# Performance work log

Hardware: AMD Instinct MI355X
Metric: run time of the kernel (lower is better)

## Reference

```python
import jax, jax.numpy as jnp
import numpy as np

B, S, E, H = 2, 2048, 1024, 16
D = E // H          # head_dim = 64
HK = H // 4         # heads per kernel group = 4
MASKED_BIAS = -10000.0


def _dwconv_causal(x, w, b):
    # x: [B, h, S, D], w: [D, k], b: [D]; causal depthwise conv along S
    k = w.shape[1]
    s = x.shape[2]
    xp = jnp.pad(x, ((0, 0), (0, 0), (k - 1, 0), (0, 0)))
    out = b
    for i in range(k):
        out = out + xp[:, :, i:i + s, :] * w[:, i]
    return out


def setup_inputs() -> dict:
    key = jax.random.key(0)
    ks = jax.random.split(key, 32)
    inp = {
        'hidden_states': jax.random.normal(ks[0], (B, S, E), jnp.float32),
        'c_attn_w': jax.random.normal(ks[1], (E, 3 * E), jnp.float32) * 0.02,
        'c_attn_b': jnp.zeros((3 * E,), jnp.float32),
        'c_proj_w': jax.random.normal(ks[2], (E, E), jnp.float32) * 0.02,
        'c_proj_b': jnp.zeros((E,), jnp.float32),
    }
    i = 3
    for pre in ('q', 'k', 'v'):
        for kern in (3, 5, 7):
            inp[f'{pre}w{kern}'] = jax.random.normal(ks[i], (D, kern), jnp.float32) * (1.0 / kern)
            inp[f'{pre}b{kern}'] = jnp.zeros((D,), jnp.float32)
            i += 1
    return inp


def _forward(hidden_states, c_attn_w, c_attn_b, c_proj_w, c_proj_b,
             qw3, qb3, qw5, qb5, qw7, qb7,
             kw3, kb3, kw5, kb5, kw7, kb7,
             vw3, vb3, vw5, vb5, vw7, vb7):
    qkv = hidden_states @ c_attn_w + c_attn_b            # [B,S,3E]
    q, k, v = jnp.split(qkv, 3, axis=-1)

    def split_heads(t):
        return t.reshape(B, S, H, D).transpose(0, 2, 1, 3)  # [B,H,S,D]

    q, k, v = split_heads(q), split_heads(k), split_heads(v)

    def tranception_mix(t, ws_bs):
        parts = [t[:, :HK]]
        for g, (w, b) in enumerate(ws_bs):
            parts.append(_dwconv_causal(t[:, (g + 1) * HK:(g + 2) * HK], w, b))
        return jnp.concatenate(parts, axis=1)

    q = tranception_mix(q, [(qw3, qb3), (qw5, qb5), (qw7, qb7)])
    k = tranception_mix(k, [(kw3, kb3), (kw5, kb5), (kw7, kb7)])
    v = tranception_mix(v, [(vw3, vb3), (vw5, vb5), (vw7, vb7)])

    scores = jnp.einsum('bhqd,bhkd->bhqk', q, k) / jnp.sqrt(jnp.float32(D))
    causal = jnp.tril(jnp.ones((S, S), bool))
    scores = jnp.where(causal, scores, jnp.float32(MASKED_BIAS))
    attn = jax.nn.softmax(scores, axis=-1)
    out = jnp.einsum('bhqk,bhkd->bhqd', attn, v)
    out = out.transpose(0, 2, 1, 3).reshape(B, S, E)
    return out @ c_proj_w + c_proj_b


def reference(hidden_states, c_attn_w, c_attn_b, c_proj_w, c_proj_b,
              qw3, qb3, qw5, qb5, qw7, qb7,
              kw3, kb3, kw5, kb5, kw7, kb7,
              vw3, vb3, vw5, vb5, vw7, vb7):
    return _forward(hidden_states, c_attn_w, c_attn_b, c_proj_w, c_proj_b,
                    qw3, qb3, qw5, qb5, qw7, qb7,
                    kw3, kb3, kw5, kb5, kw7, kb7,
                    vw3, vb3, vw5, vb5, vw7, vb7)
```

## Files before the change

kernel.cpp:

```cpp
#include <hip/hip_runtime.h>
#include <stdint.h>
#include <math.h>

typedef unsigned short u16;
typedef __attribute__((ext_vector_type(8))) short short8;
typedef __attribute__((ext_vector_type(4))) float floatx4;

#define DEV static __device__ __forceinline__

struct alignas(8) us4 { u16 x, y, z, w; };
struct alignas(16) us8 { u16 v[8]; };
struct alignas(16) f4 { float x, y, z, w; };
struct alignas(8) f2 { float x, y; };
struct alignas(8) u32x2 { uint32_t x, y; };

DEV u16 f2bf(float f) {
  uint32_t u = __float_as_uint(f);
  u += 0x7fffu + ((u >> 16) & 1u);
  return (u16)(u >> 16);
}
DEV float bf2f(u16 h) { return __uint_as_float(((uint32_t)h) << 16); }

DEV uint32_t pkbf(float a, float b) {
#if __has_builtin(__builtin_amdgcn_cvt_pk_bf16_f32)
  typedef __attribute__((ext_vector_type(2))) __bf16 bf2_t;
  bf2_t v = __builtin_amdgcn_cvt_pk_bf16_f32(a, b);
  uint32_t r; __builtin_memcpy(&r, &v, 4); return r;
#else
  return (uint32_t)f2bf(a) | ((uint32_t)f2bf(b) << 16);
#endif
}

DEV float fexp2(float x) {
#if __has_builtin(__builtin_amdgcn_exp2f)
  return __builtin_amdgcn_exp2f(x);
#else
  return exp2f(x);
#endif
}

DEV void load_lds16(const void* g, void* l) {
  __builtin_amdgcn_global_load_lds((const __attribute__((address_space(1))) void*)g,
                                   (__attribute__((address_space(3))) void*)l, 16, 0, 0);
}

__global__ __launch_bounds__(256) void prep_fused(const float* __restrict__ hidden, u16* __restrict__ h_bf,
                                                  const float* __restrict__ attn_w, u16* __restrict__ wqkvT,
                                                  const float* __restrict__ proj_w, u16* __restrict__ wprojT) {
  __shared__ float tile[32][33];
  const int bx = blockIdx.x;
  const int t = threadIdx.x;
  if (bx < 4096) {
    const int i = (bx * 256 + t) * 4;
    f4 v = *(const f4*)(hidden + i);
    us4 o; o.x = f2bf(v.x); o.y = f2bf(v.y); o.z = f2bf(v.z); o.w = f2bf(v.w);
    *(us4*)(h_bf + i) = o;
    return;
  }
  const float* in; u16* out; int K, N, n0, k0;
  if (bx < 7168) {
    const int bid = bx - 4096;
    in = attn_w; out = wqkvT; K = 1024; N = 3072;
    n0 = (bid % 96) * 32; k0 = (bid / 96) * 32;
  } else {
    const int bid = bx - 7168;
    in = proj_w; out = wprojT; K = 1024; N = 1024;
    n0 = (bid & 31) * 32; k0 = (bid >> 5) * 32;
  }
  const int tx = t & 31, ty = t >> 5;
  for (int i = ty; i < 32; i += 8)
    tile[i][tx] = in[(size_t)(k0 + i) * N + n0 + tx];
  __syncthreads();
  for (int i = ty; i < 32; i += 8)
    out[(size_t)(n0 + i) * K + k0 + tx] = f2bf(tile[tx][i]);
}

template <int EPI, int BN, int NGRP>
__global__ __launch_bounds__(256) void gemm_bt(const u16* __restrict__ A,
                                               const u16* __restrict__ Bt,
                                               const float* __restrict__ bias,
                                               void* __restrict__ outp,
                                               int M, int N, int K) {
  constexpr int NT = BN / 32;
  __shared__ u16 lA[128 * 64];
  __shared__ u16 lB[BN * 64];
  const int t = threadIdx.x;
  const int w = t >> 6, lane = t & 63;
  const int quad = lane >> 4, l15 = lane & 15;
  const int wm = w >> 1, wn = w & 1;
  const int wn_off = wn * (BN / 2);

  const int bid = blockIdx.x;
  const int gsz = 32 * NGRP;
  const int grp = bid / gsz;
  const int r = bid - grp * gsz;
  const int m0 = (r & 31) * 128;
  const int n0 = (grp * NGRP + (r >> 5)) * BN;

  floatx4 acc[4][NT] = {};

  const int srow = t >> 3;
  const int scol = (((t & 7) ^ (srow & 7)) << 3);
  const u16* gA = A + (size_t)(m0 + srow) * K + scol;
  const u16* gB = Bt + (size_t)(n0 + srow) * K + scol;
  u16* sA = lA + t * 8;
  u16* sB = lB + t * 8;
  const size_t rstep = (size_t)32 * K;

  for (int k0 = 0; k0 < K; k0 += 64) {
#pragma unroll
    for (int c = 0; c < 4; c++) load_lds16(gA + c * rstep, sA + c * 2048);
#pragma unroll
    for (int c = 0; c < BN / 32; c++) load_lds16(gB + c * rstep, sB + c * 2048);
    gA += 64; gB += 64;
    __syncthreads();
#pragma unroll
    for (int kc = 0; kc < 2; kc++) {
      short8 af[4], bfr[NT];
#pragma unroll
      for (int mt = 0; mt < 4; mt++)
        af[mt] = *(const short8*)&lA[(wm * 64 + mt * 16 + l15) * 64 + (((kc * 4 + quad) ^ (l15 & 7)) << 3)];
#pragma unroll
      for (int nt = 0; nt < NT; nt++)
        bfr[nt] = *(const short8*)&lB[(wn_off + nt * 16 + l15) * 64 + (((kc * 4 + quad) ^ (l15 & 7)) << 3)];
#pragma unroll
      for (int mt = 0; mt < 4; mt++)
#pragma unroll
        for (int nt = 0; nt < NT; nt++)
          acc[mt][nt] = __builtin_amdgcn_mfma_f32_16x16x32_bf16(bfr[nt], af[mt], acc[mt][nt], 0, 0, 0);
    }
    __syncthreads();
  }

  if (EPI == 0) {
    u16* outq = (u16*)outp;
#pragma unroll
    for (int nt = 0; nt < NT; nt++) {
      const int nb = n0 + wn_off + nt * 16 + quad * 4;
      const f4 bn4 = *(const f4*)&bias[nb];
      const int tensor = nb >> 10, e = nb & 1023;
      const int h = e >> 6, d = e & 63;
      const size_t abase = (size_t)tensor * 4194304 + (size_t)h * 131072 + d;
#pragma unroll
      for (int mt = 0; mt < 4; mt++) {
        const int rr = m0 + wm * 64 + mt * 16 + l15;
        const int b = rr >> 11, s = rr & 2047;
        u32x2 o;
        o.x = pkbf(acc[mt][nt][0] + bn4.x, acc[mt][nt][1] + bn4.y);
        o.y = pkbf(acc[mt][nt][2] + bn4.z, acc[mt][nt][3] + bn4.w);
        *(u32x2*)&outq[abase + (size_t)b * 2097152 + (size_t)s * 64] = o;
      }
    }
  } else {
    float* outf = (float*)outp;
#pragma unroll
    for (int nt = 0; nt < NT; nt++) {
      const int nb = n0 + wn_off + nt * 16 + quad * 4;
      const f4 bn4 = *(const f4*)&bias[nb];
#pragma unroll
      for (int mt = 0; mt < 4; mt++) {
        const int rr = m0 + wm * 64 + mt * 16 + l15;
        f4 o;
        o.x = acc[mt][nt][0] + bn4.x;
        o.y = acc[mt][nt][1] + bn4.y;
        o.z = acc[mt][nt][2] + bn4.z;
        o.w = acc[mt][nt][3] + bn4.w;
        *(f4*)&outf[(size_t)rr * N + nb] = o;
      }
    }
  }
}

struct ConvW { const float* w[9]; const float* b[9]; };

template <int K>
DEV void conv_run(const u16* xt, int sl0, int d, const float* wp, const float* bp,
                  float qscale, float* out32) {
  float wr[K];
#pragma unroll
  for (int j = 0; j < K; j++) wr[j] = wp[d * K + j];
  const float br = bp[d];
  float win[K];
#pragma unroll
  for (int m = 1; m < K; m++) win[m] = bf2f(xt[(sl0 + 6 - K + m) * 68 + d]);
#pragma unroll
  for (int i = 0; i < 32; i++) {
#pragma unroll
    for (int m = 0; m < K - 1; m++) win[m] = win[m + 1];
    win[K - 1] = bf2f(xt[(sl0 + 6 + i) * 68 + d]);
    float val = br;
#pragma unroll
    for (int j = 0; j < K; j++) val += wr[j] * win[j];
    out32[i] = val * qscale;
  }
}

__global__ __launch_bounds__(256) void conv_mix(const u16* __restrict__ qkv, ConvW cw,
                                                u16* __restrict__ qpost,
                                                u16* __restrict__ kpost,
                                                u16* __restrict__ vpostT) {
  __shared__ u16 xt[134 * 68];
  __shared__ u16 yt[64 * 136];
  const int t = threadIdx.x;
  const int s0 = blockIdx.x * 128;
  const int h = blockIdx.y;
  const int tz = blockIdx.z;
  const int tensor = tz >> 1, b = tz & 1;
  const u16* src = qkv + (((size_t)tensor * 2 + b) * 16 + h) * 131072;

  for (int idx = t; idx < 134 * 16; idx += 256) {
    const int row = idx >> 4, c4 = (idx & 15) << 2;
    const int s = s0 - 6 + row;
    us4 v = {0, 0, 0, 0};
    if (s >= 0) v = *(const us4*)&src[(size_t)s * 64 + c4];
    *(us4*)&xt[row * 68 + c4] = v;
  }
  __syncthreads();

  const int group = h >> 2;
  const float* wp = (group > 0) ? cw.w[tensor * 3 + group - 1] : nullptr;
  const float* bp = (group > 0) ? cw.b[tensor * 3 + group - 1] : nullptr;
  const float qscale = (tensor == 0) ? 0.18033688f : 1.0f;

  const int d = t & 63;
  const int sl0 = (t >> 6) * 32;

  float out32[32];
  if (group == 0) {
#pragma unroll
    for (int i = 0; i < 32; i++)
      out32[i] = bf2f(xt[(sl0 + 6 + i) * 68 + d]) * qscale;
  } else if (group == 1) {
    conv_run<3>(xt, sl0, d, wp, bp, qscale, out32);
  } else if (group == 2) {
    conv_run<5>(xt, sl0, d, wp, bp, qscale, out32);
  } else {
    conv_run<7>(xt, sl0, d, wp, bp, qscale, out32);
  }

  if (tensor < 2) {
    u16* outp = (tensor == 0) ? qpost : kpost;
    const size_t ob = (((size_t)b * 16 + h) * 2048 + s0) * 64;
#pragma unroll
    for (int i = 0; i < 32; i++)
      outp[ob + (size_t)(sl0 + i) * 64 + d] = f2bf(out32[i]);
  } else {
#pragma unroll
    for (int i = 0; i < 32; i++)
      yt[d * 136 + sl0 + i] = f2bf(out32[i]);
    __syncthreads();
    const size_t ob = ((size_t)b * 16 + h) * 64;
    const int sl = (t & 15) * 8;
#pragma unroll
    for (int pass = 0; pass < 4; pass++) {
      const int dd = (t >> 4) + pass * 16;
      us8 vv = *(const us8*)&yt[dd * 136 + sl];
      *(us8*)&vpostT[(ob + dd) * 2048 + s0 + sl] = vv;
    }
  }
}

static __device__ const unsigned char kOrder[24] = {
  7, 8, 10, 12, 14, 16, 18, 20, 22, 23,
  6, 21, 5, 19, 4, 17, 3, 15, 2, 13, 1, 11, 0, 9
};

__global__ __launch_bounds__(256) void attn_fwd(const u16* __restrict__ Q,
                                                const u16* __restrict__ Kp,
                                                const u16* __restrict__ Vt,
                                                u16* __restrict__ Out,
                                                u16* __restrict__ Opart,
                                                float* __restrict__ lpart) {
  __shared__ u16 lK[2][128 * 64];
  __shared__ u16 lV[2][64 * 128];
  __shared__ u16 lP[4][32 * 64];
  const int t = threadIdx.x;
  const int w = t >> 6, lane = t & 63;
  const int quad = lane >> 4, l15 = lane & 15;
  const int e7 = l15 & 7;

  const int lin = blockIdx.x;
  const int xcd = lin & 7;
  const int rest = lin >> 3;
  const int grp = rest & 3;
  const int slot = kOrder[rest >> 2];
  const int bh = grp * 8 + xcd;

  int qi, jbeg, jend, split, half;
  if (slot < 8) {
    qi = slot; jbeg = 0; jend = qi + 1; split = 0; half = 0;
  } else {
    const int k = slot - 8;
    qi = 8 + (k >> 1); half = k & 1;
    jbeg = half ? 8 : 0; jend = half ? qi + 1 : 8; split = 1;
  }

  const int b = bh >> 4, h = bh & 15;
  const size_t qkbase = (size_t)bh * 131072;
  const int qblk = qi * 128 + w * 32;

  const int krow = t >> 3;
  const int kcol = (((t & 7) ^ (krow & 7)) << 3);
  const u16* gK = Kp + qkbase + (size_t)krow * 64 + kcol;
  const int vrow = t >> 4;
  const int vcol = (((t & 15) ^ vrow) << 3);
  const u16* gV = Vt + qkbase + (size_t)vrow * 2048 + vcol;
  u16* myP = lP[w];

  short8 qf[2][2];
#pragma unroll
  for (int qt = 0; qt < 2; qt++)
#pragma unroll
    for (int kc = 0; kc < 2; kc++)
      qf[qt][kc] = *(const short8*)&Q[qkbase + (size_t)(qblk + qt * 16 + l15) * 64 + kc * 32 + quad * 8];

  {
    const int j0 = jbeg * 128;
    u16* sK = &lK[0][0] + t * 8;
    u16* sV = &lV[0][0] + t * 8;
#pragma unroll
    for (int c = 0; c < 4; c++) {
      load_lds16(gK + (size_t)(j0 + c * 32) * 64, sK + c * 2048);
      load_lds16(gV + j0 + c * 16 * 2048, sV + c * 2048);
    }
  }
  asm volatile("s_waitcnt vmcnt(0)" ::: "memory");
  __builtin_amdgcn_s_barrier();

  float lst[2] = {0.0f, 0.0f};
  floatx4 accO[4][2] = {};

  for (int j = jbeg; j < jend; ++j) {
    const int cur = (j - jbeg) & 1;

    if (j + 1 < jend) {
      const int j0n = (j + 1) * 128;
      u16* sK = &lK[cur ^ 1][0] + t * 8;
      u16* sV = &lV[cur ^ 1][0] + t * 8;
#pragma unroll
      for (int c = 0; c < 4; c++) {
        load_lds16(gK + (size_t)(j0n + c * 32) * 64, sK + c * 2048);
        load_lds16(gV + j0n + c * 16 * 2048, sV + c * 2048);
      }
    }

    const int j0 = j * 128;
    const u16* cK = lK[cur];
    const u16* cV = lV[cur];

    floatx4 accS[8][2] = {};
    __builtin_amdgcn_s_setprio(1);
#pragma unroll
    for (int kvt = 0; kvt < 8; kvt++) {
#pragma unroll
      for (int kc = 0; kc < 2; kc++) {
        const short8 a = *(const short8*)&cK[(kvt * 16 + l15) * 64 + (((kc * 4 + quad) ^ e7) << 3)];
#pragma unroll
        for (int qt = 0; qt < 2; qt++)
          accS[kvt][qt] = __builtin_amdgcn_mfma_f32_16x16x32_bf16(a, qf[qt][kc], accS[kvt][qt], 0, 0, 0);
      }
    }
    __builtin_amdgcn_s_setprio(0);

    if (j == qi) {
#pragma unroll
      for (int qt = 0; qt < 2; qt++) {
        const int q = qblk + qt * 16 + l15;
#pragma unroll
        for (int kvt = 0; kvt < 8; kvt++)
#pragma unroll
          for (int r = 0; r < 4; r++) {
            const int kv = j0 + kvt * 16 + quad * 4 + r;
            if (kv > q) accS[kvt][qt][r] = -3.0e38f;
          }
      }
    }

    uint32_t pk01[2][8], pk23[2][8];
#pragma unroll
    for (int qt = 0; qt < 2; qt++) {
      float ts = 0.0f;
#pragma unroll
      for (int kvt = 0; kvt < 8; kvt++) {
        const float p0 = fexp2(accS[kvt][qt][0]);
        const float p1 = fexp2(accS[kvt][qt][1]);
        const float p2 = fexp2(accS[kvt][qt][2]);
        const float p3 = fexp2(accS[kvt][qt][3]);
        ts += (p0 + p1) + (p2 + p3);
        pk01[qt][kvt] = pkbf(p0, p1);
        pk23[qt][kvt] = pkbf(p2, p3);
      }
      lst[qt] += ts;
    }

#pragma unroll
    for (int kvh = 0; kvh < 2; kvh++) {
#pragma unroll
      for (int qt = 0; qt < 2; qt++) {
        const int prow = (qt * 16 + l15) * 64;
#pragma unroll
        for (int kt = 0; kt < 4; kt++) {
          const int kvt = kvh * 4 + kt;
          const int slotp = (kt * 2 + (quad >> 1)) ^ e7;
          u32x2 pk; pk.x = pk01[qt][kvt]; pk.y = pk23[qt][kvt];
          *(u32x2*)&myP[prow + slotp * 8 + (quad & 1) * 4] = pk;
        }
      }
      asm volatile("s_waitcnt lgkmcnt(0)" ::: "memory");
      __builtin_amdgcn_s_setprio(1);
#pragma unroll
      for (int kk = 0; kk < 2; kk++) {
        const int kvc = kvh * 2 + kk;
        short8 pf[2];
#pragma unroll
        for (int qt = 0; qt < 2; qt++)
          pf[qt] = *(const short8*)&myP[(qt * 16 + l15) * 64 + (((kk * 4 + quad) ^ e7) << 3)];
#pragma unroll
        for (int dt = 0; dt < 4; dt++) {
          const short8 vf = *(const short8*)&cV[(dt * 16 + l15) * 128 + (((kvc * 4 + quad) ^ l15) << 3)];
#pragma unroll
          for (int qt = 0; qt < 2; qt++)
            accO[dt][qt] = __builtin_amdgcn_mfma_f32_16x16x32_bf16(vf, pf[qt], accO[dt][qt], 0, 0, 0);
        }
      }
      __builtin_amdgcn_s_setprio(0);
    }

    if (j + 1 < jend) {
      asm volatile("s_waitcnt vmcnt(0)" ::: "memory");
      __builtin_amdgcn_s_barrier();
    }
  }

#pragma unroll
  for (int qt = 0; qt < 2; qt++) {
    lst[qt] += __shfl_xor(lst[qt], 16);
    lst[qt] += __shfl_xor(lst[qt], 32);
  }

  if (!split) {
#pragma unroll
    for (int qt = 0; qt < 2; qt++) {
      const float inv = 1.0f / lst[qt];
      const int q = qblk + qt * 16 + l15;
#pragma unroll
      for (int dt = 0; dt < 4; dt++) {
        u32x2 o;
        o.x = pkbf(accO[dt][qt][0] * inv, accO[dt][qt][1] * inv);
        o.y = pkbf(accO[dt][qt][2] * inv, accO[dt][qt][3] * inv);
        *(u32x2*)&Out[((size_t)b * 2048 + q) * 1024 + h * 64 + dt * 16 + quad * 4] = o;
      }
    }
  } else {
    const int pidx = (bh * 8 + (qi - 8)) * 2 + half;
    u16* op = Opart + (size_t)pidx * 8192;
#pragma unroll
    for (int qt = 0; qt < 2; qt++) {
      const int ql = w * 32 + qt * 16 + l15;
#pragma unroll
      for (int dt = 0; dt < 4; dt++) {
        u32x2 o;
        o.x = pkbf(accO[dt][qt][0], accO[dt][qt][1]);
        o.y = pkbf(accO[dt][qt][2], accO[dt][qt][3]);
        *(u32x2*)&op[(size_t)ql * 64 + dt * 16 + quad * 4] = o;
      }
      if (quad == 0) lpart[pidx * 128 + ql] = lst[qt];
    }
  }
}

__global__ __launch_bounds__(256) void attn_reduce(const u16* __restrict__ Opart,
                                                   const float* __restrict__ lpart,
                                                   u16* __restrict__ Out) {
  const int qr = blockIdx.x;
  const int bh = blockIdx.y;
  const int b = bh >> 4, h = bh & 15;
  const int t = threadIdx.x;
  const int row = t >> 1, dh = (t & 1) * 32;
  const int pbase = (bh * 8 + qr) * 2;

  const float l1 = lpart[pbase * 128 + row];
  const float l2 = lpart[(pbase + 1) * 128 + row];
  const float inv = 1.0f / (l1 + l2);

  const u16* s1 = Opart + ((size_t)pbase * 128 + row) * 64 + dh;
  const u16* s2 = Opart + ((size_t)(pbase + 1) * 128 + row) * 64 + dh;
  u16* dst = Out + ((size_t)b * 2048 + (8 + qr) * 128 + row) * 1024 + h * 64 + dh;
#pragma unroll
  for (int i = 0; i < 4; i++) {
    us8 v1 = *(const us8*)&s1[i * 8];
    us8 v2 = *(const us8*)&s2[i * 8];
    float o[8];
#pragma unroll
    for (int e = 0; e < 8; e++) o[e] = (bf2f(v1.v[e]) + bf2f(v2.v[e])) * inv;
    u32x2 lo; lo.x = pkbf(o[0], o[1]); lo.y = pkbf(o[2], o[3]);
    u32x2 hi; hi.x = pkbf(o[4], o[5]); hi.y = pkbf(o[6], o[7]);
    *(u32x2*)&dst[i * 8] = lo;
    *(u32x2*)&dst[i * 8 + 4] = hi;
  }
}

extern "C" void kernel_launch(void* const* d_in, const int* in_sizes, int n_in,
                              void* d_out, int out_size, void* d_ws, size_t ws_size,
                              hipStream_t stream) {
  (void)in_sizes; (void)n_in; (void)out_size; (void)ws_size;
  const float* hidden = (const float*)d_in[0];
  const float* attn_w = (const float*)d_in[1];
  const float* attn_b = (const float*)d_in[2];
  const float* proj_w = (const float*)d_in[3];
  const float* proj_b = (const float*)d_in[4];
  ConvW cw;
  for (int i = 0; i < 9; i++) {
    cw.w[i] = (const float*)d_in[5 + 2 * i];
    cw.b[i] = (const float*)d_in[6 + 2 * i];
  }

  uint8_t* ws = (uint8_t*)d_ws;
  u16* h_bf   = (u16*)(ws + 0);
  u16* wqkvT  = (u16*)(ws + 8388608);
  u16* qkvpre = (u16*)(ws + 14680064);
  u16* qpost  = (u16*)(ws + 39845888);
  u16* kpost  = (u16*)(ws + 48234496);
  u16* vpostT = (u16*)(ws + 56623104);
  u16* attno  = (u16*)(ws + 65011712);
  u16* wprojT = (u16*)(ws + 73400320);
  u16* Opart  = (u16*)(ws + 0);
  float* lpart = (float*)(ws + 8388608);

  prep_fused<<<8192, 256, 0, stream>>>(hidden, h_bf, attn_w, wqkvT, proj_w, wprojT);
  gemm_bt<0, 128, 6><<<768, 256, 0, stream>>>(h_bf, wqkvT, attn_b, (void*)qkvpre, 4096, 3072, 1024);
  conv_mix<<<dim3(16, 16, 6), 256, 0, stream>>>(qkvpre, cw, qpost, kpost, vpostT);
  attn_fwd<<<dim3(768), 256, 0, stream>>>(qpost, kpost, vpostT, attno, Opart, lpart);
  attn_reduce<<<dim3(8, 32), 256, 0, stream>>>(Opart, lpart, attno);
  gemm_bt<1, 64, 8><<<512, 256, 0, stream>>>(attno, wprojT, proj_b, d_out, 4096, 1024, 1024);
}
```

Measured before the change: 236.7 us.

## Add dedicated 256x256-tile QKV GEMM with double-buffered direct-to-LDS loads

Replaces the generic QKV projection GEMM with a specialized kernel using 256x256 output tiles, 512 threads (8 waves), and a 128 KB LDS double buffer. Global-to-LDS loads of the next K tile are interleaved across MFMA phases, and s_setprio raises priority around the MFMA bursts. The larger tile is meant to improve operand reuse and hide memory latency. In exchange the grid drops to 192 blocks, which may underfill the MI355X CUs, and LDS use rises sharply.

```diff
diff --git a/kernel.cpp b/kernel.cpp
--- a/kernel.cpp
+++ b/kernel.cpp
@@ -73,6 +73,118 @@
   __syncthreads();
   for (int i = ty; i < 32; i += 8)
     out[(size_t)(n0 + i) * K + k0 + tx] = f2bf(tile[tx][i]);
+}
+
+__global__ __launch_bounds__(512) void gemm_qkv(const u16* __restrict__ A,
+                                                const u16* __restrict__ Bt,
+                                                const float* __restrict__ bias,
+                                                u16* __restrict__ outq) {
+  constexpr int K = 1024;
+  __shared__ u16 lds[65536];
+  const int t = threadIdx.x;
+  const int w = t >> 6, lane = t & 63;
+  const int quad = lane >> 4, l15 = lane & 15;
+  const int wm = w >> 2, wn = w & 3;
+
+  const int bid = blockIdx.x;
+  const int m0 = (bid & 15) * 256;
+  const int n0 = (bid >> 4) * 256;
+
+  floatx4 acc[8][4] = {};
+
+  const int srow = t >> 3;
+  const int schunk = (t & 7) ^ (srow & 7);
+  const u16* gA0 = A + (size_t)(m0 + srow) * K + schunk * 8;
+  const u16* gB0 = Bt + (size_t)(n0 + srow) * K + schunk * 8;
+  const size_t rstep = (size_t)64 * K;
+
+#pragma unroll
+  for (int r = 0; r < 4; r++) {
+    load_lds16(gA0 + r * rstep, lds + r * 4096 + t * 8);
+    load_lds16(gB0 + r * rstep, lds + 16384 + r * 4096 + t * 8);
+  }
+  asm volatile("s_waitcnt vmcnt(0)" ::: "memory");
+  __builtin_amdgcn_s_barrier();
+
+#pragma unroll 1
+  for (int kt = 0; kt < 16; ++kt) {
+    const int b = kt & 1;
+    const u16* cA = lds + b * 32768;
+    const u16* cB = lds + b * 32768 + 16384;
+    const int last = (kt == 15);
+
+#pragma unroll
+    for (int phase = 0; phase < 4; ++phase) {
+      const int mh = phase >> 1, nh = phase & 1;
+
+      short8 aF[4][2], bF[2][2];
+#pragma unroll
+      for (int mi = 0; mi < 4; mi++) {
+        const int row = wm * 128 + mh * 64 + mi * 16 + l15;
+#pragma unroll
+        for (int kk = 0; kk < 2; kk++)
+          aF[mi][kk] = *(const short8*)&cA[row * 64 + (((kk * 4 + quad) ^ (row & 7)) << 3)];
+      }
+#pragma unroll
+      for (int ni = 0; ni < 2; ni++) {
+        const int rowb = wn * 64 + nh * 32 + ni * 16 + l15;
+#pragma unroll
+        for (int kk = 0; kk < 2; kk++)
+          bF[ni][kk] = *(const short8*)&cB[rowb * 64 + (((kk * 4 + quad) ^ (rowb & 7)) << 3)];
+      }
+
+      if (!last) {
+        u16* dbuf = lds + (b ^ 1) * 32768;
+        const size_t koff = (size_t)(kt + 1) * 64;
+        if (phase == 0) {
+#pragma unroll
+          for (int r = 0; r < 4; r++)
+            load_lds16(gA0 + r * rstep + koff, dbuf + r * 4096 + t * 8);
+        } else if (phase == 1) {
+#pragma unroll
+          for (int r = 0; r < 4; r++)
+            load_lds16(gB0 + r * rstep + koff, dbuf + 16384 + r * 4096 + t * 8);
+        }
+      }
+
+      asm volatile("" ::: "memory");
+      __builtin_amdgcn_s_barrier();
+
+      __builtin_amdgcn_s_setprio(1);
+#pragma unroll
+      for (int mi = 0; mi < 4; mi++)
+#pragma unroll
+        for (int ni = 0; ni < 2; ni++)
+#pragma unroll
+          for (int kk = 0; kk < 2; kk++)
+            acc[mh * 4 + mi][nh * 2 + ni] =
+                __builtin_amdgcn_mfma_f32_16x16x32_bf16(bF[ni][kk], aF[mi][kk],
+                                                        acc[mh * 4 + mi][nh * 2 + ni], 0, 0, 0);
+      __builtin_amdgcn_s_setprio(0);
+
+      if (phase == 3 && !last) asm volatile("s_waitcnt vmcnt(0)" ::: "memory");
+      asm volatile("" ::: "memory");
+      __builtin_amdgcn_s_barrier();
+    }
+  }
+
+#pragma unroll
+  for (int ni2 = 0; ni2 < 4; ni2++) {
+    const int nb = n0 + wn * 64 + ni2 * 16 + quad * 4;
+    const f4 bn4 = *(const f4*)&bias[nb];
+    const int tensor = nb >> 10, e = nb & 1023;
+    const int h = e >> 6, d = e & 63;
+    const size_t abase = (size_t)tensor * 4194304 + (size_t)h * 131072 + d;
+#pragma unroll
+    for (int mi2 = 0; mi2 < 8; mi2++) {
+      const int rr = m0 + wm * 128 + mi2 * 16 + l15;
+      const int bb = rr >> 11, s = rr & 2047;
+      u32x2 o;
+      o.x = pkbf(acc[mi2][ni2][0] + bn4.x, acc[mi2][ni2][1] + bn4.y);
+      o.y = pkbf(acc[mi2][ni2][2] + bn4.z, acc[mi2][ni2][3] + bn4.w);
+      *(u32x2*)&outq[abase + (size_t)bb * 2097152 + (size_t)s * 64] = o;
+    }
+  }
 }
 
 template <int EPI, int BN, int NGRP>
@@ -528,7 +640,7 @@
   float* lpart = (float*)(ws + 8388608);
 
   prep_fused<<<8192, 256, 0, stream>>>(hidden, h_bf, attn_w, wqkvT, proj_w, wprojT);
-  gemm_bt<0, 128, 6><<<768, 256, 0, stream>>>(h_bf, wqkvT, attn_b, (void*)qkvpre, 4096, 3072, 1024);
+  gemm_qkv<<<dim3(192), 512, 0, stream>>>(h_bf, wqkvT, attn_b, qkvpre);
   conv_mix<<<dim3(16, 16, 6), 256, 0, stream>>>(qkvpre, cw, qpost, kpost, vpostT);
   attn_fwd<<<dim3(768), 256, 0, stream>>>(qpost, kpost, vpostT, attno, Opart, lpart);
   attn_reduce<<<dim3(8, 32), 256, 0, stream>>>(Opart, lpart, attno);
```

New measurement: 239.9 us. About the same (+1.3%).
